# Performance work log

Measured on AMD Instinct MI355X. Metric: run time of the kernel, lower is better.

The kernel has to match this reference:

```python
import jax, jax.numpy as jnp
import numpy as np

D_MODEL = 1024
NUM_HEADS = 16
D_K = D_MODEL // NUM_HEADS

def setup_inputs() -> dict:
    key = jax.random.key(0)
    ks = jax.random.split(key, 8)
    B, S, D = 2, 2048, D_MODEL
    scale = 1.0 / np.sqrt(D)
    return {
        "X_q": jax.random.normal(ks[0], (B, S, D), dtype=jnp.float32),
        "X_k": jax.random.normal(ks[1], (B, S, D), dtype=jnp.float32),
        "X_v": jax.random.normal(ks[2], (B, S, D), dtype=jnp.float32),
        "W_q": jax.random.normal(ks[3], (D, D), dtype=jnp.float32) * scale,
        "W_k": jax.random.normal(ks[4], (D, D), dtype=jnp.float32) * scale,
        "W_v": jax.random.normal(ks[5], (D, D), dtype=jnp.float32) * scale,
        "W_o": jax.random.normal(ks[6], (D, D), dtype=jnp.float32) * scale,
        "b_o": jnp.zeros((D,), dtype=jnp.float32),
    }

def reference(X_q, X_k, X_v, W_q, W_k, W_v, W_o, b_o):
    B, S, D = X_q.shape
    H, dk = NUM_HEADS, D_K
    # nn.Linear: x @ W.T
    Q = (X_q @ W_q.T).reshape(B, H, S, dk)  # faithful raw view, no transpose
    K = (X_k @ W_k.T).reshape(B, H, S, dk)
    V = (X_v @ W_v.T).reshape(B, H, S, dk)
    A = jnp.einsum("bhqd,bhkd->bhqk", Q, K) / np.sqrt(dk)  # [B,H,S,S]
    A = jax.nn.softmax(A, axis=-1)
    H_cat = jnp.einsum("bhqk,bhkd->bhqd", A, V).reshape(B, S, D)
    return H_cat @ W_o.T + b_o
```

## Files before the change

### kernel.cpp

```cpp
#include <hip/hip_runtime.h>

typedef __bf16 bf16;
typedef bf16 bf16x8 __attribute__((ext_vector_type(8)));
typedef bf16 bf16x4 __attribute__((ext_vector_type(4)));
typedef float f32x4 __attribute__((ext_vector_type(4)));

#define XSZ 4194304
#define WSZ 1048576
#define KDIM 1024

__device__ __forceinline__ void async16(const bf16* g, bf16* l) {
  __builtin_amdgcn_global_load_lds(
      (const __attribute__((address_space(1))) unsigned int*)g,
      (__attribute__((address_space(3))) unsigned int*)l, 16, 0, 0);
}

__device__ __forceinline__ bf16x8 ld8(const bf16* p) {
  bf16x4 lo = *(const bf16x4*)p;
  bf16x4 hi = *(const bf16x4*)(p + 4);
  return __builtin_shufflevector(lo, hi, 0, 1, 2, 3, 4, 5, 6, 7);
}

__device__ __forceinline__ void st8s(bf16* p, bf16x8 v) {
  *(bf16x4*)p       = __builtin_shufflevector(v, v, 0, 1, 2, 3);
  *(bf16x4*)(p + 4) = __builtin_shufflevector(v, v, 4, 5, 6, 7);
}

__device__ __forceinline__ f32x4 mfma16(bf16x8 a, bf16x8 b, f32x4 c) {
  return __builtin_amdgcn_mfma_f32_16x16x32_bf16(a, b, c, 0, 0, 0);
}

__global__ __launch_bounds__(256) void cast_bf16(const float* __restrict__ src,
                                                 bf16* __restrict__ dst, int n, float scale) {
  int i = (blockIdx.x * 256 + threadIdx.x) * 8;
  if (i >= n) return;
  float4 a = *(const float4*)(src + i);
  float4 b = *(const float4*)(src + i + 4);
  bf16x8 o;
  o[0] = (bf16)(a.x * scale); o[1] = (bf16)(a.y * scale);
  o[2] = (bf16)(a.z * scale); o[3] = (bf16)(a.w * scale);
  o[4] = (bf16)(b.x * scale); o[5] = (bf16)(b.y * scale);
  o[6] = (bf16)(b.z * scale); o[7] = (bf16)(b.w * scale);
  *(bf16x8*)(dst + i) = o;
}

__device__ __forceinline__ void gemm_nt_core(const bf16* __restrict__ A, const bf16* __restrict__ Bm,
                                             int m0, int n0, bf16* lds, f32x4 acc[4][4]) {
  const int t = threadIdx.x;
  const int lane = t & 63, wave = t >> 6;
  const int wm = wave & 1, wn = wave >> 1;
  const int quad = lane >> 4, m16 = lane & 15;
  bf16* As = lds;
  bf16* Bs = lds + 128 * 32;
  const int c0 = t, c1 = t + 256;
  const bf16* ga0 = A + (size_t)(m0 + (c0 >> 2)) * KDIM + (c0 & 3) * 8;
  const bf16* ga1 = A + (size_t)(m0 + (c1 >> 2)) * KDIM + (c1 & 3) * 8;
  const bf16* gb0 = Bm + (size_t)(n0 + (c0 >> 2)) * KDIM + (c0 & 3) * 8;
  const bf16* gb1 = Bm + (size_t)(n0 + (c1 >> 2)) * KDIM + (c1 & 3) * 8;
  for (int kt = 0; kt < KDIM; kt += 32) {
    async16(ga0 + kt, As + c0 * 8);
    async16(ga1 + kt, As + c1 * 8);
    async16(gb0 + kt, Bs + c0 * 8);
    async16(gb1 + kt, Bs + c1 * 8);
    __syncthreads();
    bf16x8 af[4], bfv[4];
    #pragma unroll
    for (int i = 0; i < 4; i++)
      af[i] = *(const bf16x8*)(As + (wm * 64 + i * 16 + m16) * 32 + quad * 8);
    #pragma unroll
    for (int i = 0; i < 4; i++)
      bfv[i] = *(const bf16x8*)(Bs + (wn * 64 + i * 16 + m16) * 32 + quad * 8);
    #pragma unroll
    for (int mi = 0; mi < 4; mi++)
      #pragma unroll
      for (int ni = 0; ni < 4; ni++)
        acc[mi][ni] = mfma16(af[mi], bfv[ni], acc[mi][ni]);
    __syncthreads();
  }
}

__global__ __launch_bounds__(256) void proj_gemm(const bf16* __restrict__ xq, const bf16* __restrict__ xk,
                                                 const bf16* __restrict__ xv, const bf16* __restrict__ wq,
                                                 const bf16* __restrict__ wk, const bf16* __restrict__ wv,
                                                 bf16* __restrict__ Qo, bf16* __restrict__ Ko,
                                                 bf16* __restrict__ Vo) {
  __shared__ bf16 lds[2 * 128 * 32];
  const int z = blockIdx.z;
  const bf16* A = (z == 0) ? xq : (z == 1) ? xk : xv;
  const bf16* W = (z == 0) ? wq : (z == 1) ? wk : wv;
  bf16* C = (z == 0) ? Qo : (z == 1) ? Ko : Vo;
  f32x4 acc[4][4];
  #pragma unroll
  for (int i = 0; i < 4; i++)
    #pragma unroll
    for (int j = 0; j < 4; j++) acc[i][j] = (f32x4){0.f, 0.f, 0.f, 0.f};
  gemm_nt_core(A, W, blockIdx.y * 128, blockIdx.x * 128, lds, acc);
  const int lane = threadIdx.x & 63, wave = threadIdx.x >> 6;
  const int wm = wave & 1, wn = wave >> 1, quad = lane >> 4, m16 = lane & 15;
  const int row0 = blockIdx.y * 128 + wm * 64;
  const int col0 = blockIdx.x * 128 + wn * 64;
  #pragma unroll
  for (int mi = 0; mi < 4; mi++)
    #pragma unroll
    for (int ni = 0; ni < 4; ni++)
      #pragma unroll
      for (int r = 0; r < 4; r++) {
        int row = row0 + mi * 16 + quad * 4 + r;
        int col = col0 + ni * 16 + m16;
        C[(size_t)row * 1024 + col] = (bf16)acc[mi][ni][r];
      }
}

__global__ __launch_bounds__(256) void out_gemm(const bf16* __restrict__ Hm, const bf16* __restrict__ wo,
                                                const float* __restrict__ bias, float* __restrict__ out) {
  __shared__ bf16 lds[2 * 128 * 32];
  f32x4 acc[4][4];
  #pragma unroll
  for (int i = 0; i < 4; i++)
    #pragma unroll
    for (int j = 0; j < 4; j++) acc[i][j] = (f32x4){0.f, 0.f, 0.f, 0.f};
  gemm_nt_core(Hm, wo, blockIdx.y * 128, blockIdx.x * 128, lds, acc);
  const int lane = threadIdx.x & 63, wave = threadIdx.x >> 6;
  const int wm = wave & 1, wn = wave >> 1, quad = lane >> 4, m16 = lane & 15;
  const int row0 = blockIdx.y * 128 + wm * 64;
  const int col0 = blockIdx.x * 128 + wn * 64;
  float bv[4];
  #pragma unroll
  for (int ni = 0; ni < 4; ni++) bv[ni] = bias[col0 + ni * 16 + m16];
  #pragma unroll
  for (int mi = 0; mi < 4; mi++)
    #pragma unroll
    for (int ni = 0; ni < 4; ni++)
      #pragma unroll
      for (int r = 0; r < 4; r++) {
        int row = row0 + mi * 16 + quad * 4 + r;
        int col = col0 + ni * 16 + m16;
        out[(size_t)row * 1024 + col] = acc[mi][ni][r] + bv[ni];
      }
}

__global__ __launch_bounds__(256) void transpose_v(const bf16* __restrict__ V, bf16* __restrict__ Vt) {
  __shared__ bf16 T[64 * 65];
  const int t = threadIdx.x;
  const bf16* src = V + (size_t)blockIdx.y * (2048 * 64) + (size_t)blockIdx.x * 64 * 64;
  bf16* dst = Vt + (size_t)blockIdx.y * (2048 * 64) + (size_t)blockIdx.x * 64;
  #pragma unroll
  for (int j = 0; j < 2; j++) {
    int c = t + j * 256;
    int row = c >> 3, col8 = (c & 7) * 8;
    bf16x8 v = *(const bf16x8*)(src + row * 64 + col8);
    #pragma unroll
    for (int i = 0; i < 8; i++) T[row * 65 + col8 + i] = v[i];
  }
  __syncthreads();
  #pragma unroll
  for (int j = 0; j < 2; j++) {
    int c = t + j * 256;
    int d = c >> 3, k8 = (c & 7) * 8;
    bf16x8 o;
    #pragma unroll
    for (int i = 0; i < 8; i++) o[i] = T[(k8 + i) * 65 + d];
    *(bf16x8*)(dst + (size_t)d * 2048 + k8) = o;
  }
}

#define KS_STRIDE 68
#define PS_STRIDE 132
#define VS_STRIDE 132
#define KP_ELEMS (128 * PS_STRIDE)

__global__ __launch_bounds__(256, 2) void attn_kernel(const bf16* __restrict__ Qg,
                                                      const bf16* __restrict__ Kg,
                                                      const bf16* __restrict__ Vtg,
                                                      bf16* __restrict__ Og) {
  __shared__ bf16 smem[KP_ELEMS + 64 * VS_STRIDE];
  bf16* KsPs = smem;
  bf16* Vs = smem + KP_ELEMS;
  const int t = threadIdx.x;
  const int lane = t & 63, wave = t >> 6;
  const int quad = lane >> 4, m16 = lane & 15;
  const size_t base = (size_t)blockIdx.y * (2048 * 64);
  const bf16* Qp = Qg + base + (size_t)blockIdx.x * 128 * 64;
  const bf16* Kp = Kg + base;
  const bf16* Vp = Vtg + base;

  bf16x8 qf[2][2];
  #pragma unroll
  for (int mi = 0; mi < 2; mi++)
    #pragma unroll
    for (int kc = 0; kc < 2; kc++)
      qf[mi][kc] = *(const bf16x8*)(Qp + (size_t)(wave * 32 + mi * 16 + m16) * 64 + kc * 32 + quad * 8);

  f32x4 oacc[2][4];
  #pragma unroll
  for (int mi = 0; mi < 2; mi++)
    #pragma unroll
    for (int nd = 0; nd < 4; nd++) oacc[mi][nd] = (f32x4){0.f, 0.f, 0.f, 0.f};
  float mrow[2][4], lrow[2][4];
  #pragma unroll
  for (int mi = 0; mi < 2; mi++)
    #pragma unroll
    for (int r = 0; r < 4; r++) { mrow[mi][r] = -INFINITY; lrow[mi][r] = 0.f; }

  for (int kt = 0; kt < 2048; kt += 128) {
    #pragma unroll
    for (int j = 0; j < 4; j++) {
      int c = t + j * 256;
      int row = c >> 3, col8 = (c & 7) * 8;
      bf16x8 v = *(const bf16x8*)(Kp + (size_t)(kt + row) * 64 + col8);
      st8s(KsPs + row * KS_STRIDE + col8, v);
    }
    #pragma unroll
    for (int j = 0; j < 4; j++) {
      int c = t + j * 256;
      int d = c >> 4, col8 = (c & 15) * 8;
      bf16x8 v = *(const bf16x8*)(Vp + (size_t)d * 2048 + kt + col8);
      st8s(Vs + d * VS_STRIDE + col8, v);
    }
    __syncthreads();

    f32x4 sacc[2][8];
    #pragma unroll
    for (int mi = 0; mi < 2; mi++)
      #pragma unroll
      for (int ni = 0; ni < 8; ni++) sacc[mi][ni] = (f32x4){0.f, 0.f, 0.f, 0.f};
    #pragma unroll
    for (int kc = 0; kc < 2; kc++) {
      bf16x8 kf[8];
      #pragma unroll
      for (int ni = 0; ni < 8; ni++)
        kf[ni] = ld8(KsPs + (ni * 16 + m16) * KS_STRIDE + kc * 32 + quad * 8);
      #pragma unroll
      for (int mi = 0; mi < 2; mi++)
        #pragma unroll
        for (int ni = 0; ni < 8; ni++)
          sacc[mi][ni] = mfma16(qf[mi][kc], kf[ni], sacc[mi][ni]);
    }
    __syncthreads();

    #pragma unroll
    for (int mi = 0; mi < 2; mi++) {
      #pragma unroll
      for (int r = 0; r < 4; r++) {
        float mx = sacc[mi][0][r];
        #pragma unroll
        for (int ni = 1; ni < 8; ni++) mx = fmaxf(mx, sacc[mi][ni][r]);
        #pragma unroll
        for (int s = 1; s < 16; s <<= 1) mx = fmaxf(mx, __shfl_xor(mx, s, 64));
        float mold = mrow[mi][r];
        float mnew = fmaxf(mold, mx);
        float a = __expf(mold - mnew);
        int qrow = wave * 32 + mi * 16 + quad * 4 + r;
        float sum = 0.f;
        #pragma unroll
        for (int ni = 0; ni < 8; ni++) {
          float p = __expf(sacc[mi][ni][r] - mnew);
          sum += p;
          KsPs[qrow * PS_STRIDE + ni * 16 + m16] = (bf16)p;
        }
        #pragma unroll
        for (int s = 1; s < 16; s <<= 1) sum += __shfl_xor(sum, s, 64);
        lrow[mi][r] = lrow[mi][r] * a + sum;
        mrow[mi][r] = mnew;
        #pragma unroll
        for (int nd = 0; nd < 4; nd++) oacc[mi][nd][r] *= a;
      }
    }

    #pragma unroll
    for (int kc = 0; kc < 4; kc++) {
      bf16x8 pf[2], vf[4];
      #pragma unroll
      for (int mi = 0; mi < 2; mi++)
        pf[mi] = ld8(KsPs + (wave * 32 + mi * 16 + m16) * PS_STRIDE + kc * 32 + quad * 8);
      #pragma unroll
      for (int nd = 0; nd < 4; nd++)
        vf[nd] = ld8(Vs + (nd * 16 + m16) * VS_STRIDE + kc * 32 + quad * 8);
      #pragma unroll
      for (int mi = 0; mi < 2; mi++)
        #pragma unroll
        for (int nd = 0; nd < 4; nd++)
          oacc[mi][nd] = mfma16(pf[mi], vf[nd], oacc[mi][nd]);
    }
    __syncthreads();
  }

  #pragma unroll
  for (int mi = 0; mi < 2; mi++)
    #pragma unroll
    for (int r = 0; r < 4; r++) {
      float inv = 1.f / lrow[mi][r];
      int q = blockIdx.x * 128 + wave * 32 + mi * 16 + quad * 4 + r;
      #pragma unroll
      for (int nd = 0; nd < 4; nd++)
        Og[base + (size_t)q * 64 + nd * 16 + m16] = (bf16)(oacc[mi][nd][r] * inv);
    }
}

extern "C" void kernel_launch(void* const* d_in, const int* in_sizes, int n_in,
                              void* d_out, int out_size, void* d_ws, size_t ws_size,
                              hipStream_t stream) {
  const float* Xq = (const float*)d_in[0];
  const float* Xk = (const float*)d_in[1];
  const float* Xv = (const float*)d_in[2];
  const float* Wq = (const float*)d_in[3];
  const float* Wk = (const float*)d_in[4];
  const float* Wv = (const float*)d_in[5];
  const float* Wo = (const float*)d_in[6];
  const float* bo = (const float*)d_in[7];

  bf16* ws = (bf16*)d_ws;
  bf16* xq = ws;
  bf16* xk = ws + XSZ;
  bf16* xv = ws + 2 * (size_t)XSZ;
  bf16* wq = ws + 3 * (size_t)XSZ;
  bf16* wk = wq + WSZ;
  bf16* wv = wk + WSZ;
  bf16* wo = wv + WSZ;
  bf16* q  = wo + WSZ;
  bf16* k  = q + XSZ;
  bf16* v  = k + XSZ;
  bf16* vt = xv;
  bf16* h  = xq;

  cast_bf16<<<XSZ / 2048, 256, 0, stream>>>(Xq, xq, XSZ, 1.0f);
  cast_bf16<<<XSZ / 2048, 256, 0, stream>>>(Xk, xk, XSZ, 1.0f);
  cast_bf16<<<XSZ / 2048, 256, 0, stream>>>(Xv, xv, XSZ, 1.0f);
  cast_bf16<<<WSZ / 2048, 256, 0, stream>>>(Wq, wq, WSZ, 0.125f);
  cast_bf16<<<WSZ / 2048, 256, 0, stream>>>(Wk, wk, WSZ, 1.0f);
  cast_bf16<<<WSZ / 2048, 256, 0, stream>>>(Wv, wv, WSZ, 1.0f);
  cast_bf16<<<WSZ / 2048, 256, 0, stream>>>(Wo, wo, WSZ, 1.0f);

  proj_gemm<<<dim3(8, 32, 3), 256, 0, stream>>>(xq, xk, xv, wq, wk, wv, q, k, v);
  transpose_v<<<dim3(32, 32), 256, 0, stream>>>(v, vt);
  attn_kernel<<<dim3(16, 32), 256, 0, stream>>>(q, k, vt, h);
  out_gemm<<<dim3(8, 32), 256, 0, stream>>>(h, wo, bo, (float*)d_out);
}
```

Baseline: 278.4 us.

## Rewrite attention with 32x32 MFMA, register-resident P, exp2 softmax; fuse casts

The attention kernel now uses 32x32x16 MFMA tiles and computes S transposed (K as A operand), so each lane owns one query row. P is passed to the PV MFMA through registers with cross-half lane shuffles rather than a round trip through shared memory. That removes the P LDS buffer, one barrier per tile, and the 16-lane shuffle reductions. Softmax uses exp2 with log2e folded into the Q weight scale, and the seven cast launches are merged into one kernel. In exchange, register pressure rises and the cast kernel gains per-thread branching.

```diff
diff --git a/kernel.cpp b/kernel.cpp
--- a/kernel.cpp
+++ b/kernel.cpp
@@ -3,11 +3,15 @@
 typedef __bf16 bf16;
 typedef bf16 bf16x8 __attribute__((ext_vector_type(8)));
 typedef bf16 bf16x4 __attribute__((ext_vector_type(4)));
+typedef bf16 bf16x2 __attribute__((ext_vector_type(2)));
 typedef float f32x4 __attribute__((ext_vector_type(4)));
+typedef float f32x16 __attribute__((ext_vector_type(16)));
+typedef int i32x4 __attribute__((ext_vector_type(4)));
 
 #define XSZ 4194304
 #define WSZ 1048576
 #define KDIM 1024
+#define QSCALE 0.1803368801111137f
 
 __device__ __forceinline__ void async16(const bf16* g, bf16* l) {
   __builtin_amdgcn_global_load_lds(
@@ -29,13 +33,30 @@
 __device__ __forceinline__ f32x4 mfma16(bf16x8 a, bf16x8 b, f32x4 c) {
   return __builtin_amdgcn_mfma_f32_16x16x32_bf16(a, b, c, 0, 0, 0);
 }
-
-__global__ __launch_bounds__(256) void cast_bf16(const float* __restrict__ src,
-                                                 bf16* __restrict__ dst, int n, float scale) {
-  int i = (blockIdx.x * 256 + threadIdx.x) * 8;
-  if (i >= n) return;
-  float4 a = *(const float4*)(src + i);
-  float4 b = *(const float4*)(src + i + 4);
+__device__ __forceinline__ f32x16 mfma32(bf16x8 a, bf16x8 b, f32x16 c) {
+  return __builtin_amdgcn_mfma_f32_32x32x16_bf16(a, b, c, 0, 0, 0);
+}
+
+__device__ __forceinline__ int packbf2(float lo, float hi) {
+  bf16x2 t; t[0] = (bf16)lo; t[1] = (bf16)hi;
+  return __builtin_bit_cast(int, t);
+}
+
+__global__ __launch_bounds__(256) void cast_all(const float* __restrict__ Xq, const float* __restrict__ Xk,
+                                                const float* __restrict__ Xv, const float* __restrict__ Wq,
+                                                const float* __restrict__ Wk, const float* __restrict__ Wv,
+                                                const float* __restrict__ Wo, bf16* __restrict__ dst) {
+  size_t i = ((size_t)blockIdx.x * 256 + threadIdx.x) * 8;
+  const float* src; size_t off; float scale = 1.0f;
+  if (i < XSZ)                { src = Xq; off = i; }
+  else if (i < 2 * (size_t)XSZ) { src = Xk; off = i - XSZ; }
+  else if (i < 3 * (size_t)XSZ) { src = Xv; off = i - 2 * (size_t)XSZ; }
+  else if (i < 3 * (size_t)XSZ + WSZ) { src = Wq; off = i - 3 * (size_t)XSZ; scale = QSCALE; }
+  else if (i < 3 * (size_t)XSZ + 2 * (size_t)WSZ) { src = Wk; off = i - 3 * (size_t)XSZ - WSZ; }
+  else if (i < 3 * (size_t)XSZ + 3 * (size_t)WSZ) { src = Wv; off = i - 3 * (size_t)XSZ - 2 * (size_t)WSZ; }
+  else                        { src = Wo; off = i - 3 * (size_t)XSZ - 3 * (size_t)WSZ; }
+  float4 a = *(const float4*)(src + off);
+  float4 b = *(const float4*)(src + off + 4);
   bf16x8 o;
   o[0] = (bf16)(a.x * scale); o[1] = (bf16)(a.y * scale);
   o[2] = (bf16)(a.z * scale); o[3] = (bf16)(a.w * scale);
@@ -164,136 +185,122 @@
   }
 }
 
-#define KS_STRIDE 68
-#define PS_STRIDE 132
-#define VS_STRIDE 132
-#define KP_ELEMS (128 * PS_STRIDE)
-
+#define KS 68
+#define VS 132
 __global__ __launch_bounds__(256, 2) void attn_kernel(const bf16* __restrict__ Qg,
                                                       const bf16* __restrict__ Kg,
                                                       const bf16* __restrict__ Vtg,
                                                       bf16* __restrict__ Og) {
-  __shared__ bf16 smem[KP_ELEMS + 64 * VS_STRIDE];
-  bf16* KsPs = smem;
-  bf16* Vs = smem + KP_ELEMS;
+  __shared__ bf16 smem[128 * KS + 64 * VS];
+  bf16* Ks = smem;
+  bf16* Vs = smem + 128 * KS;
   const int t = threadIdx.x;
-  const int lane = t & 63, wave = t >> 6;
-  const int quad = lane >> 4, m16 = lane & 15;
+  const int lane = t & 63, w = t >> 6;
+  const int l31 = lane & 31, h = lane >> 5;
   const size_t base = (size_t)blockIdx.y * (2048 * 64);
-  const bf16* Qp = Qg + base + (size_t)blockIdx.x * 128 * 64;
   const bf16* Kp = Kg + base;
   const bf16* Vp = Vtg + base;
-
-  bf16x8 qf[2][2];
-  #pragma unroll
-  for (int mi = 0; mi < 2; mi++)
-    #pragma unroll
-    for (int kc = 0; kc < 2; kc++)
-      qf[mi][kc] = *(const bf16x8*)(Qp + (size_t)(wave * 32 + mi * 16 + m16) * 64 + kc * 32 + quad * 8);
-
-  f32x4 oacc[2][4];
-  #pragma unroll
-  for (int mi = 0; mi < 2; mi++)
-    #pragma unroll
-    for (int nd = 0; nd < 4; nd++) oacc[mi][nd] = (f32x4){0.f, 0.f, 0.f, 0.f};
-  float mrow[2][4], lrow[2][4];
-  #pragma unroll
-  for (int mi = 0; mi < 2; mi++)
-    #pragma unroll
-    for (int r = 0; r < 4; r++) { mrow[mi][r] = -INFINITY; lrow[mi][r] = 0.f; }
+  const int q = blockIdx.x * 128 + w * 32 + l31;
+
+  bf16x8 qf[4];
+  #pragma unroll
+  for (int kc = 0; kc < 4; kc++)
+    qf[kc] = *(const bf16x8*)(Qg + base + (size_t)q * 64 + 16 * kc + 8 * h);
+
+  f32x16 oacc[2];
+  #pragma unroll
+  for (int mt = 0; mt < 2; mt++)
+    #pragma unroll
+    for (int i = 0; i < 16; i++) oacc[mt][i] = 0.f;
+  float mrow = -INFINITY, lrow = 0.f;
 
   for (int kt = 0; kt < 2048; kt += 128) {
     #pragma unroll
     for (int j = 0; j < 4; j++) {
       int c = t + j * 256;
       int row = c >> 3, col8 = (c & 7) * 8;
-      bf16x8 v = *(const bf16x8*)(Kp + (size_t)(kt + row) * 64 + col8);
-      st8s(KsPs + row * KS_STRIDE + col8, v);
+      st8s(Ks + row * KS + col8, *(const bf16x8*)(Kp + (size_t)(kt + row) * 64 + col8));
     }
     #pragma unroll
     for (int j = 0; j < 4; j++) {
       int c = t + j * 256;
       int d = c >> 4, col8 = (c & 15) * 8;
-      bf16x8 v = *(const bf16x8*)(Vp + (size_t)d * 2048 + kt + col8);
-      st8s(Vs + d * VS_STRIDE + col8, v);
+      st8s(Vs + d * VS + col8, *(const bf16x8*)(Vp + (size_t)d * 2048 + kt + col8));
     }
     __syncthreads();
 
-    f32x4 sacc[2][8];
-    #pragma unroll
-    for (int mi = 0; mi < 2; mi++)
-      #pragma unroll
-      for (int ni = 0; ni < 8; ni++) sacc[mi][ni] = (f32x4){0.f, 0.f, 0.f, 0.f};
-    #pragma unroll
-    for (int kc = 0; kc < 2; kc++) {
-      bf16x8 kf[8];
-      #pragma unroll
-      for (int ni = 0; ni < 8; ni++)
-        kf[ni] = ld8(KsPs + (ni * 16 + m16) * KS_STRIDE + kc * 32 + quad * 8);
-      #pragma unroll
-      for (int mi = 0; mi < 2; mi++)
-        #pragma unroll
-        for (int ni = 0; ni < 8; ni++)
-          sacc[mi][ni] = mfma16(qf[mi][kc], kf[ni], sacc[mi][ni]);
-    }
-    __syncthreads();
-
-    #pragma unroll
-    for (int mi = 0; mi < 2; mi++) {
-      #pragma unroll
-      for (int r = 0; r < 4; r++) {
-        float mx = sacc[mi][0][r];
-        #pragma unroll
-        for (int ni = 1; ni < 8; ni++) mx = fmaxf(mx, sacc[mi][ni][r]);
-        #pragma unroll
-        for (int s = 1; s < 16; s <<= 1) mx = fmaxf(mx, __shfl_xor(mx, s, 64));
-        float mold = mrow[mi][r];
-        float mnew = fmaxf(mold, mx);
-        float a = __expf(mold - mnew);
-        int qrow = wave * 32 + mi * 16 + quad * 4 + r;
-        float sum = 0.f;
-        #pragma unroll
-        for (int ni = 0; ni < 8; ni++) {
-          float p = __expf(sacc[mi][ni][r] - mnew);
-          sum += p;
-          KsPs[qrow * PS_STRIDE + ni * 16 + m16] = (bf16)p;
-        }
-        #pragma unroll
-        for (int s = 1; s < 16; s <<= 1) sum += __shfl_xor(sum, s, 64);
-        lrow[mi][r] = lrow[mi][r] * a + sum;
-        mrow[mi][r] = mnew;
-        #pragma unroll
-        for (int nd = 0; nd < 4; nd++) oacc[mi][nd][r] *= a;
-      }
-    }
-
-    #pragma unroll
-    for (int kc = 0; kc < 4; kc++) {
-      bf16x8 pf[2], vf[4];
-      #pragma unroll
-      for (int mi = 0; mi < 2; mi++)
-        pf[mi] = ld8(KsPs + (wave * 32 + mi * 16 + m16) * PS_STRIDE + kc * 32 + quad * 8);
-      #pragma unroll
-      for (int nd = 0; nd < 4; nd++)
-        vf[nd] = ld8(Vs + (nd * 16 + m16) * VS_STRIDE + kc * 32 + quad * 8);
-      #pragma unroll
-      for (int mi = 0; mi < 2; mi++)
-        #pragma unroll
-        for (int nd = 0; nd < 4; nd++)
-          oacc[mi][nd] = mfma16(pf[mi], vf[nd], oacc[mi][nd]);
+    f32x16 sacc[4];
+    #pragma unroll
+    for (int mt = 0; mt < 4; mt++)
+      #pragma unroll
+      for (int i = 0; i < 16; i++) sacc[mt][i] = 0.f;
+    #pragma unroll
+    for (int mt = 0; mt < 4; mt++)
+      #pragma unroll
+      for (int kc = 0; kc < 4; kc++) {
+        bf16x8 kf = ld8(Ks + (32 * mt + l31) * KS + 16 * kc + 8 * h);
+        sacc[mt] = mfma32(kf, qf[kc], sacc[mt]);
+      }
+
+    float mx = sacc[0][0];
+    #pragma unroll
+    for (int mt = 0; mt < 4; mt++)
+      #pragma unroll
+      for (int i = 0; i < 16; i++) mx = fmaxf(mx, sacc[mt][i]);
+    mx = fmaxf(mx, __shfl_xor(mx, 32, 64));
+    float mnew = fmaxf(mrow, mx);
+    float a = exp2f(mrow - mnew);
+    float sum = 0.f;
+    int pd[4][8];
+    #pragma unroll
+    for (int mt = 0; mt < 4; mt++)
+      #pragma unroll
+      for (int p = 0; p < 8; p++) {
+        float p0 = exp2f(sacc[mt][2 * p] - mnew);
+        float p1 = exp2f(sacc[mt][2 * p + 1] - mnew);
+        sum += p0 + p1;
+        pd[mt][p] = packbf2(p0, p1);
+      }
+    sum += __shfl_xor(sum, 32, 64);
+    lrow = lrow * a + sum;
+    mrow = mnew;
+    #pragma unroll
+    for (int mt = 0; mt < 2; mt++)
+      #pragma unroll
+      for (int i = 0; i < 16; i++) oacc[mt][i] *= a;
+
+    #pragma unroll
+    for (int kc = 0; kc < 8; kc++) {
+      const int mts = kc >> 1, c1 = kc & 1;
+      const int rro = 2 * c1 + h;
+      const int rrp = 2 * c1 + 1 - h;
+      int s0 = __shfl_xor(pd[mts][2 * rrp], 32, 64);
+      int s1 = __shfl_xor(pd[mts][2 * rrp + 1], 32, 64);
+      int o0 = pd[mts][2 * rro], o1 = pd[mts][2 * rro + 1];
+      i32x4 w4;
+      w4.x = h ? s0 : o0;
+      w4.y = h ? s1 : o1;
+      w4.z = h ? o0 : s0;
+      w4.w = h ? o1 : s1;
+      bf16x8 pfrag = __builtin_bit_cast(bf16x8, w4);
+      #pragma unroll
+      for (int mtd = 0; mtd < 2; mtd++) {
+        bf16x8 vf = ld8(Vs + (32 * mtd + l31) * VS + 16 * kc + 8 * h);
+        oacc[mtd] = mfma32(vf, pfrag, oacc[mtd]);
+      }
     }
     __syncthreads();
   }
 
-  #pragma unroll
-  for (int mi = 0; mi < 2; mi++)
-    #pragma unroll
-    for (int r = 0; r < 4; r++) {
-      float inv = 1.f / lrow[mi][r];
-      int q = blockIdx.x * 128 + wave * 32 + mi * 16 + quad * 4 + r;
-      #pragma unroll
-      for (int nd = 0; nd < 4; nd++)
-        Og[base + (size_t)q * 64 + nd * 16 + m16] = (bf16)(oacc[mi][nd][r] * inv);
+  float inv = 1.f / lrow;
+  #pragma unroll
+  for (int mt = 0; mt < 2; mt++)
+    #pragma unroll
+    for (int r2 = 0; r2 < 4; r2++) {
+      bf16x4 ov;
+      #pragma unroll
+      for (int i = 0; i < 4; i++) ov[i] = (bf16)(oacc[mt][4 * r2 + i] * inv);
+      *(bf16x4*)(Og + base + (size_t)q * 64 + 32 * mt + 8 * r2 + 4 * h) = ov;
     }
 }
 
@@ -323,14 +330,7 @@
   bf16* vt = xv;
   bf16* h  = xq;
 
-  cast_bf16<<<XSZ / 2048, 256, 0, stream>>>(Xq, xq, XSZ, 1.0f);
-  cast_bf16<<<XSZ / 2048, 256, 0, stream>>>(Xk, xk, XSZ, 1.0f);
-  cast_bf16<<<XSZ / 2048, 256, 0, stream>>>(Xv, xv, XSZ, 1.0f);
-  cast_bf16<<<WSZ / 2048, 256, 0, stream>>>(Wq, wq, WSZ, 0.125f);
-  cast_bf16<<<WSZ / 2048, 256, 0, stream>>>(Wk, wk, WSZ, 1.0f);
-  cast_bf16<<<WSZ / 2048, 256, 0, stream>>>(Wv, wv, WSZ, 1.0f);
-  cast_bf16<<<WSZ / 2048, 256, 0, stream>>>(Wo, wo, WSZ, 1.0f);
-
+  cast_all<<<8192, 256, 0, stream>>>(Xq, Xk, Xv, Wq, Wk, Wv, Wo, ws);
   proj_gemm<<<dim3(8, 32, 3), 256, 0, stream>>>(xq, xk, xv, wq, wk, wv, q, k, v);
   transpose_v<<<dim3(32, 32), 256, 0, stream>>>(v, vt);
   attn_kernel<<<dim3(16, 32), 256, 0, stream>>>(q, k, vt, h);
```

After: 286.7 us. +3.0%, slower.
